# Kernel tuning notes

Hardware: AMD Instinct MI355X
Metric: run time of the kernel (lower is better)

## Reference

```python
import jax, jax.numpy as jnp
import numpy as np

B, N, V, E_PER = 64, 512, 64, 16384
IN, H, OUT = 128, 256, 10
TOTAL_N = B * N
E = B * E_PER


def _lin_init(key, fan_in, fan_out):
    return jax.random.normal(key, (fan_in, fan_out), jnp.float32) * (1.0 / np.sqrt(fan_in))


def setup_inputs() -> dict:
    key = jax.random.key(0)
    ks = jax.random.split(key, 16)
    x = jax.random.normal(ks[0], (TOTAL_N, IN), jnp.float32)
    # within-graph random edges, offset to global node ids
    off = (jnp.arange(B, dtype=jnp.int32) * N)[:, None]
    edge_src = (jax.random.randint(ks[1], (B, E_PER), 0, N, dtype=jnp.int32) + off).reshape(-1)
    edge_dst = (jax.random.randint(ks[2], (B, E_PER), 0, N, dtype=jnp.int32) + off).reshape(-1)
    inp = dict(
        x=x, edge_src=edge_src, edge_dst=edge_dst,
        W_emb=_lin_init(ks[3], IN, H), b_emb=jnp.zeros((H,), jnp.float32),
        W_gcn=_lin_init(ks[4], H, H), b_gcn=jnp.zeros((H,), jnp.float32),
        aW1=_lin_init(ks[5], H, H), ab1=jnp.zeros((H,), jnp.float32),
        aW2=_lin_init(ks[6], H, H), ab2=jnp.zeros((H,), jnp.float32),
        vW1=_lin_init(ks[7], H, H), vb1=jnp.zeros((H,), jnp.float32),
        vW2=_lin_init(ks[8], H, H), vb2=jnp.zeros((H,), jnp.float32),
        mW1=_lin_init(ks[9], H, H), mb1=jnp.zeros((H,), jnp.float32),
        mW2=_lin_init(ks[10], H, OUT), mb2=jnp.zeros((OUT,), jnp.float32),
        edge_weights=jnp.ones((B, N, V), jnp.float32) / V,  # uniform init
    )
    return inp


def reference(x, edge_src, edge_dst, W_emb, b_emb, W_gcn, b_gcn,
              aW1, ab1, aW2, ab2, vW1, vb1, vW2, vb2,
              mW1, mb1, mW2, mb2, edge_weights):
    # node embedding
    h = x @ W_emb + b_emb                                   # [BN, H]
    # GCNConv with symmetric normalization + self loops (PyG semantics)
    hw = h @ W_gcn                                          # [BN, H]
    deg = 1.0 + jax.ops.segment_sum(jnp.ones((E,), jnp.float32), edge_dst, num_segments=TOTAL_N)
    dinv = jax.lax.rsqrt(deg)
    coef = (dinv[edge_src] * dinv[edge_dst])[:, None]
    agg = jax.ops.segment_sum(hw[edge_src] * coef, edge_dst, num_segments=TOTAL_N)
    agg = agg + hw / deg[:, None]                           # self-loop term (norm = 1/deg)
    h = jax.nn.relu(agg + b_gcn)
    g = h.reshape(B, N, H)                                  # per-graph node features
    # affinity MLP + cosine similarity to graph prototype
    t = jax.nn.relu(g @ aW1 + ab1) @ aW2 + ab2              # [B, N, H]
    proto = t.mean(axis=1)                                  # [B, H]
    eps = 1e-8
    tn = jnp.maximum(jnp.linalg.norm(t, axis=-1), eps)      # [B, N]
    pn = jnp.maximum(jnp.linalg.norm(proto, axis=-1), eps)  # [B]
    sim = jnp.einsum('bnh,bh->bn', t, proto) / (tn * pn[:, None])
    att = 0.5 * (1.0 + sim)                                 # [B, N]
    mw = edge_weights * att[:, :, None]                     # [B, N, V]
    rs = mw.sum(axis=-1, keepdims=True)
    mw = mw / jnp.where(rs == 0.0, 1.0, rs)                 # row-normalize (top_k=None path)
    # weighted scatter of node features into virtual nodes
    vn = jnp.einsum('bnv,bnh->bvh', mw, g)                  # [B, V, H]
    vn = jax.nn.relu(vn @ vW1 + vb1) @ vW2 + vb2
    gf = vn.mean(axis=1)                                    # [B, H]
    out = jax.nn.relu(gf @ mW1 + mb1) @ mW2 + mb2           # [B, OUT]
    return out
```

## Files before the change

kernel.cpp:

```cpp
#include <hip/hip_runtime.h>
#include <hip/hip_bf16.h>

#define DEVINL __device__ __forceinline__

typedef unsigned short u16;
typedef short v8s   __attribute__((ext_vector_type(8)));
typedef float v4f   __attribute__((ext_vector_type(4)));
typedef u16   v4u16 __attribute__((ext_vector_type(4)));
typedef short v4s16 __attribute__((ext_vector_type(4)));

constexpr int Bg      = 64;
constexpr int Nn      = 512;
constexpr int Vv      = 64;
constexpr int IND     = 128;
constexpr int Hd      = 256;
constexpr int OUTD    = 10;
constexpr int TOTAL_N = Bg * Nn;
constexpr int NE      = Bg * 16384;
constexpr int E_PER   = 16384;

DEVINL u16 f2bf(float f) {
    unsigned u = __float_as_uint(f);
    u += 0x7FFF + ((u >> 16) & 1);
    return (u16)(u >> 16);
}
DEVINL float bf2f(u16 s) { return __uint_as_float(((unsigned)s) << 16); }

DEVINL void ld4f(const float* p, float o[4]) {
    float4 v = *(const float4*)p;
    o[0] = v.x; o[1] = v.y; o[2] = v.z; o[3] = v.w;
}
DEVINL void ld4f(const u16* p, float o[4]) {
    v4u16 v = *(const v4u16*)p;
    o[0] = bf2f(v[0]); o[1] = bf2f(v[1]); o[2] = bf2f(v[2]); o[3] = bf2f(v[3]);
}
DEVINL void stC(float* C, size_t idx, float v) { C[idx] = v; }
DEVINL void stC(u16* C, size_t idx, float v)   { C[idx] = f2bf(v); }

__global__ __launch_bounds__(1024) void k_csr(const int* __restrict__ esrc,
                                              const int* __restrict__ edst,
                                              int2* __restrict__ csr,
                                              int* __restrict__ rowstart,
                                              float* __restrict__ dinv) {
    __shared__ int   cnt[512];
    __shared__ int   cur[512];
    __shared__ float dv[512];
    int g = blockIdx.x;
    int tid = threadIdx.x;
    if (tid < 512) cnt[tid] = 0;
    __syncthreads();
    const int base = g * E_PER;
#pragma unroll
    for (int i = 0; i < E_PER / 1024; i++) {
        int d = edst[base + i * 1024 + tid];
        atomicAdd(&cnt[d & 511], 1);
    }
    __syncthreads();
    if (tid < 512) cur[tid] = cnt[tid];
    __syncthreads();
    for (int off = 1; off < 512; off <<= 1) {
        int v = 0;
        if (tid < 512 && tid >= off) v = cur[tid - off];
        __syncthreads();
        if (tid < 512) cur[tid] += v;
        __syncthreads();
    }
    if (tid < 512) {
        int excl = cur[tid] - cnt[tid];
        rowstart[g * 512 + tid] = base + excl;
        float di = rsqrtf((float)(cnt[tid] + 1));
        dv[tid] = di;
        dinv[g * 512 + tid] = di;
        cur[tid] = excl;
    }
    if (g == 0 && tid == 0) rowstart[TOTAL_N] = NE;
    __syncthreads();
#pragma unroll
    for (int i = 0; i < E_PER / 1024; i++) {
        int e = base + i * 1024 + tid;
        int s = esrc[e], d = edst[e];
        int sl = s & 511, dl = d & 511;
        int pos = atomicAdd(&cur[dl], 1);
        int2 rec;
        rec.x = s;
        rec.y = __float_as_int(dv[sl] * dv[dl]);
        csr[base + pos] = rec;
    }
}

struct WtArgs {
    const float* src[5];
    u16* dst[5];
};
__global__ __launch_bounds__(256) void k_wt(WtArgs a) {
    int bid = blockIdx.x;
    int mi = bid / 16, tile = bid % 16;
    int k0 = (tile & 3) * 64, n0 = (tile >> 2) * 64;
    const float* src = a.src[mi];
    u16* dst = a.dst[mi];
    __shared__ float T[64][65];
    int t = threadIdx.x;
#pragma unroll
    for (int j = 0; j < 16; j++) {
        int idx = t + 256 * j;
        int r = idx >> 6, c = idx & 63;
        T[c][r] = src[(size_t)(k0 + r) * 256 + n0 + c];
    }
    __syncthreads();
#pragma unroll
    for (int j = 0; j < 16; j++) {
        int idx = t + 256 * j;
        int nr = idx >> 6, kc = idx & 63;
        dst[(size_t)(n0 + nr) * 256 + k0 + kc] = f2bf(T[nr][kc]);
    }
}

__global__ __launch_bounds__(256) void k_b12(const float* __restrict__ b_emb,
                                             const float* __restrict__ W_gcn,
                                             float* __restrict__ b12) {
    int t = threadIdx.x;
    float acc = 0.f;
    for (int k = 0; k < IND; k++) acc += b_emb[k] * W_gcn[(size_t)k * 256 + t];
    b12[t] = acc;
}

template <typename TA, typename TC>
__global__ __launch_bounds__(256) void k_mfma_gemm(const TA* __restrict__ A,
                                                   const u16* __restrict__ Wt,
                                                   const float* __restrict__ bias,
                                                   const float* __restrict__ srow,
                                                   const float* __restrict__ b12v,
                                                   TC* __restrict__ C,
                                                   int M, int K, int relu, int tstore) {
    constexpr int LDK = 88;
    __shared__ short As[128 * LDK];
    __shared__ short Bs[128 * LDK];
    int tid  = threadIdx.x;
    int row0 = blockIdx.y * 128, col0 = blockIdx.x * 128;
    int lane = tid & 63, wid = tid >> 6;
    int wm = (wid >> 1) * 64, wn = (wid & 1) * 64;
    int q = lane >> 4, r = lane & 15;
    v4f acc[4][4];
#pragma unroll
    for (int i = 0; i < 4; i++)
#pragma unroll
        for (int j = 0; j < 4; j++) acc[i][j] = (v4f){0.f, 0.f, 0.f, 0.f};
    int sm = tid >> 1, sk = (tid & 1) * 32;
    for (int k0 = 0; k0 < K; k0 += 64) {
        const TA* ap  = A  + (size_t)(row0 + sm) * K + k0 + sk;
        const u16* bp = Wt + (size_t)(col0 + sm) * K + k0 + sk;
        short* adst = &As[sm * LDK + sk];
        short* bdst = &Bs[sm * LDK + sk];
#pragma unroll
        for (int i = 0; i < 8; i++) {
            float o[4];
            ld4f(ap + 4 * i, o);
            v4s16 pa;
            pa[0] = (short)f2bf(o[0]); pa[1] = (short)f2bf(o[1]);
            pa[2] = (short)f2bf(o[2]); pa[3] = (short)f2bf(o[3]);
            *(v4s16*)(adst + 4 * i) = pa;
            *(v4u16*)(bdst + 4 * i) = *(const v4u16*)(bp + 4 * i);
        }
        __syncthreads();
#pragma unroll
        for (int ks = 0; ks < 64; ks += 32) {
            v8s af[4], bfr[4];
#pragma unroll
            for (int i = 0; i < 4; i++)
                af[i] = *(const v8s*)&As[(wm + i * 16 + r) * LDK + ks + q * 8];
#pragma unroll
            for (int j = 0; j < 4; j++)
                bfr[j] = *(const v8s*)&Bs[(wn + j * 16 + r) * LDK + ks + q * 8];
#pragma unroll
            for (int i = 0; i < 4; i++)
#pragma unroll
                for (int j = 0; j < 4; j++)
                    acc[i][j] = __builtin_amdgcn_mfma_f32_16x16x32_bf16(af[i], bfr[j], acc[i][j], 0, 0, 0);
        }
        __syncthreads();
    }
#pragma unroll
    for (int i = 0; i < 4; i++) {
#pragma unroll
        for (int j = 0; j < 4; j++) {
            int col = col0 + wn + j * 16 + r;
            float bcol = bias ? bias[col] : 0.f;
            float b12c = b12v ? b12v[col] : 0.f;
#pragma unroll
            for (int rg = 0; rg < 4; rg++) {
                int row = row0 + wm + i * 16 + q * 4 + rg;
                float v = acc[i][j][rg] + bcol;
                if (srow) v += srow[row] * b12c;
                if (relu) v = fmaxf(v, 0.f);
                if (tstore) stC(C, (size_t)col * M + row, v);
                else        stC(C, (size_t)row * 256 + col, v);
            }
        }
    }
}

__global__ __launch_bounds__(128) void k_aggx(const float* __restrict__ x,
                                              const int* __restrict__ rowstart,
                                              const int2* __restrict__ csr,
                                              const float* __restrict__ dinv,
                                              float* __restrict__ xa,
                                              float* __restrict__ s) {
    __shared__ int2 lrec[128];
    int node = ((blockIdx.x & 7) << 12) | (blockIdx.x >> 3);
    int ch = threadIdx.x;
    float di = dinv[node];
    float invdeg = di * di;
    float acc = x[(size_t)node * IND + ch] * invdeg;
    float ssum = invdeg;
    int rs0 = rowstart[node], rs1 = rowstart[node + 1];
    for (int base = rs0; base < rs1; base += 128) {
        int e = base + ch;
        if (e < rs1) lrec[ch] = csr[e];
        __syncthreads();
        int m = min(128, rs1 - base);
        for (int i = 0; i < m; i++) {
            int2 rr = lrec[i];
            float c = __int_as_float(rr.y);
            acc += x[(size_t)rr.x * IND + ch] * c;
            ssum += c;
        }
        __syncthreads();
    }
    xa[(size_t)node * IND + ch] = acc;
    if (ch == 0) s[node] = ssum;
}

__global__ __launch_bounds__(1024) void k_proto(const u16* __restrict__ t,
                                                float* __restrict__ proto,
                                                float* __restrict__ pn) {
    __shared__ float part[4][256];
    __shared__ float red[256];
    int b = blockIdx.x;
    int tid = threadIdx.x;
    int st = tid >> 8, ch = tid & 255;
    float sm = 0.f;
    int n0 = st * 128;
    for (int n = n0; n < n0 + 128; n++)
        sm += bf2f(t[(size_t)(b * Nn + n) * Hd + ch]);
    part[st][ch] = sm;
    __syncthreads();
    if (tid < 256) {
        float p = (part[0][ch] + part[1][ch] + part[2][ch] + part[3][ch]) * (1.f / (float)Nn);
        proto[b * Hd + ch] = p;
        red[ch] = p * p;
    }
    __syncthreads();
    for (int off = 128; off > 0; off >>= 1) {
        if (tid < off) red[tid] += red[tid + off];
        __syncthreads();
    }
    if (tid == 0) pn[b] = fmaxf(sqrtf(red[0]), 1e-8f);
}

__global__ __launch_bounds__(256) void k_att(const u16* __restrict__ t,
                                             const float* __restrict__ proto,
                                             const float* __restrict__ pn,
                                             const float* __restrict__ ew,
                                             float* __restrict__ scale) {
    int tid = threadIdx.x;
    int lane = tid & 63, widx = tid >> 6;
    int node = blockIdx.x * 4 + widx;
    int b = node >> 9;
    v4u16 tv4 = *(const v4u16*)&t[(size_t)node * Hd + lane * 4];
    float4 pv4 = *(const float4*)&proto[b * Hd + lane * 4];
    float t0 = bf2f(tv4[0]), t1 = bf2f(tv4[1]), t2 = bf2f(tv4[2]), t3 = bf2f(tv4[3]);
    float dot = t0 * pv4.x + t1 * pv4.y + t2 * pv4.z + t3 * pv4.w;
    float sq  = t0 * t0 + t1 * t1 + t2 * t2 + t3 * t3;
    float wv  = ew[(size_t)node * Vv + lane];
#pragma unroll
    for (int off = 32; off > 0; off >>= 1) {
        dot += __shfl_xor(dot, off);
        sq  += __shfl_xor(sq, off);
        wv  += __shfl_xor(wv, off);
    }
    if (lane == 0) {
        float tn  = fmaxf(sqrtf(sq), 1e-8f);
        float sim = dot / (tn * pn[b]);
        float att = 0.5f * (1.f + sim);
        float rs  = att * wv;
        float den = (rs == 0.f) ? 1.f : rs;
        scale[node] = att / den;
    }
}

constexpr int LDV = 36;
DEVINL v8s ld_frag36(const short* p) {
    v4s16 lo = *(const v4s16*)p;
    v4s16 hi = *(const v4s16*)(p + 4);
    v8s f;
    f[0] = lo[0]; f[1] = lo[1]; f[2] = lo[2]; f[3] = lo[3];
    f[4] = hi[0]; f[5] = hi[1]; f[6] = hi[2]; f[7] = hi[3];
    return f;
}
__global__ __launch_bounds__(256) void k_vn_mfma(const float* __restrict__ ew,
                                                 const float* __restrict__ scale,
                                                 const u16* __restrict__ g,
                                                 u16* __restrict__ vn) {
    __shared__ short As[64 * LDV];
    __shared__ short Bs[256 * LDV];
    int b = blockIdx.x;
    int tid = threadIdx.x;
    int lane = tid & 63, wid = tid >> 6;
    int h0 = wid * 64;
    int q = lane >> 4, r = lane & 15;
    v4f acc[4][4];
#pragma unroll
    for (int i = 0; i < 4; i++)
#pragma unroll
        for (int j = 0; j < 4; j++) acc[i][j] = (v4f){0.f, 0.f, 0.f, 0.f};
    for (int k0 = 0; k0 < Nn; k0 += 32) {
#pragma unroll
        for (int p = 0; p < 8; p++) {
            int e = tid + 256 * p;
            int nl = e >> 6, v = e & 63;
            int n = b * Nn + k0 + nl;
            As[v * LDV + nl] = (short)f2bf(ew[(size_t)n * Vv + v] * scale[n]);
        }
#pragma unroll
        for (int p = 0; p < 8; p++) {
            int e = tid + 256 * p;
            int h = e & 255, kgrp = e >> 8;
            int kl = kgrp * 4;
            v4s16 tmp;
#pragma unroll
            for (int c = 0; c < 4; c++)
                tmp[c] = (short)g[(size_t)(b * Nn + k0 + kl + c) * Hd + h];
            *(v4s16*)&Bs[h * LDV + kl] = tmp;
        }
        __syncthreads();
        v8s af[4], bfr[4];
#pragma unroll
        for (int i = 0; i < 4; i++)
            af[i] = ld_frag36(&As[(i * 16 + r) * LDV + q * 8]);
#pragma unroll
        for (int j = 0; j < 4; j++)
            bfr[j] = ld_frag36(&Bs[(h0 + j * 16 + r) * LDV + q * 8]);
#pragma unroll
        for (int i = 0; i < 4; i++)
#pragma unroll
            for (int j = 0; j < 4; j++)
                acc[i][j] = __builtin_amdgcn_mfma_f32_16x16x32_bf16(af[i], bfr[j], acc[i][j], 0, 0, 0);
        __syncthreads();
    }
#pragma unroll
    for (int i = 0; i < 4; i++)
#pragma unroll
        for (int j = 0; j < 4; j++) {
            int col = h0 + j * 16 + r;
#pragma unroll
            for (int rg = 0; rg < 4; rg++) {
                int v = i * 16 + q * 4 + rg;
                vn[(size_t)(b * Vv + v) * Hd + col] = f2bf(acc[i][j][rg]);
            }
        }
}

__global__ __launch_bounds__(256) void k_head(const float* __restrict__ vn2,
                                              const float* __restrict__ mW1,
                                              const float* __restrict__ mb1,
                                              const float* __restrict__ mW2,
                                              const float* __restrict__ mb2,
                                              float* __restrict__ out) {
    __shared__ float gfs[256];
    __shared__ float zs[256];
    int b = blockIdx.x, t = threadIdx.x;
    float s = 0.f;
    for (int v = 0; v < Vv; v++) s += vn2[(size_t)(b * Vv + v) * Hd + t];
    gfs[t] = s * (1.f / (float)Vv);
    __syncthreads();
    float z = mb1[t];
    for (int k = 0; k < Hd; k++) z += gfs[k] * mW1[k * Hd + t];
    zs[t] = fmaxf(z, 0.f);
    __syncthreads();
    if (t < OUTD) {
        float o = mb2[t];
        for (int ch = 0; ch < Hd; ch++) o += zs[ch] * mW2[ch * OUTD + t];
        out[b * OUTD + t] = o;
    }
}

extern "C" void kernel_launch(void* const* d_in, const int* in_sizes, int n_in,
                              void* d_out, int out_size, void* d_ws, size_t ws_size,
                              hipStream_t stream) {
    const float* x     = (const float*)d_in[0];
    const int*   esrc  = (const int*)d_in[1];
    const int*   edst  = (const int*)d_in[2];
    const float* W_emb = (const float*)d_in[3];
    const float* b_emb = (const float*)d_in[4];
    const float* W_gcn = (const float*)d_in[5];
    const float* b_gcn = (const float*)d_in[6];
    const float* aW1   = (const float*)d_in[7];
    const float* ab1   = (const float*)d_in[8];
    const float* aW2   = (const float*)d_in[9];
    const float* ab2   = (const float*)d_in[10];
    const float* vW1   = (const float*)d_in[11];
    const float* vb1   = (const float*)d_in[12];
    const float* vW2   = (const float*)d_in[13];
    const float* vb2   = (const float*)d_in[14];
    const float* mW1   = (const float*)d_in[15];
    const float* mb1   = (const float*)d_in[16];
    const float* mW2   = (const float*)d_in[17];
    const float* mb2   = (const float*)d_in[18];
    const float* ew    = (const float*)d_in[19];
    float* out = (float*)d_out;

    char* w = (char*)d_ws;
    auto alloc = [&](size_t bytes) -> void* {
        void* p = (void*)w;
        w += (bytes + 255) & ~(size_t)255;
        return p;
    };
    int*   rowstart = (int*)  alloc((TOTAL_N + 1) * 4);
    float* dinv     = (float*)alloc(TOTAL_N * 4);
    int2*  csr      = (int2*) alloc((size_t)NE * 8);
    float* xa       = (float*)alloc((size_t)TOTAL_N * IND * 4);
    float* srow     = (float*)alloc(TOTAL_N * 4);
    u16*   g_bf     = (u16*)  alloc((size_t)TOTAL_N * Hd * 2);
    u16*   t1_bf    = (u16*)  alloc((size_t)TOTAL_N * Hd * 2);
    u16*   t_bf     = (u16*)  alloc((size_t)TOTAL_N * Hd * 2);
    u16*   vn_bf    = (u16*)  alloc((size_t)Bg * Vv * Hd * 2);
    u16*   vtmp_bf  = (u16*)  alloc((size_t)Bg * Vv * Hd * 2);
    float* vn2      = (float*)alloc((size_t)Bg * Vv * Hd * 4);
    float* proto    = (float*)alloc(Bg * Hd * 4);
    float* pn       = (float*)alloc(Bg * 4);
    float* scale    = (float*)alloc(TOTAL_N * 4);
    float* b12      = (float*)alloc(Hd * 4);
    u16*   wt_gcn   = (u16*)  alloc((size_t)Hd * Hd * 2);
    u16*   wt_a1    = (u16*)  alloc((size_t)Hd * Hd * 2);
    u16*   wt_a2    = (u16*)  alloc((size_t)Hd * Hd * 2);
    u16*   wt_v1    = (u16*)  alloc((size_t)Hd * Hd * 2);
    u16*   wt_v2    = (u16*)  alloc((size_t)Hd * Hd * 2);
    u16*   wt_12    = (u16*)  alloc((size_t)Hd * IND * 2);

    WtArgs wa;
    wa.src[0] = W_gcn; wa.dst[0] = wt_gcn;
    wa.src[1] = aW1;   wa.dst[1] = wt_a1;
    wa.src[2] = aW2;   wa.dst[2] = wt_a2;
    wa.src[3] = vW1;   wa.dst[3] = wt_v1;
    wa.src[4] = vW2;   wa.dst[4] = wt_v2;
    k_wt<<<80, 256, 0, stream>>>(wa);

    k_mfma_gemm<float, u16><<<dim3(2, 1), 256, 0, stream>>>(
        W_emb, wt_gcn, nullptr, nullptr, nullptr, wt_12, IND, Hd, 0, 1);
    k_b12<<<1, 256, 0, stream>>>(b_emb, W_gcn, b12);

    k_csr<<<Bg, 1024, 0, stream>>>(esrc, edst, csr, rowstart, dinv);

    k_aggx<<<TOTAL_N, 128, 0, stream>>>(x, rowstart, csr, dinv, xa, srow);

    k_mfma_gemm<float, u16><<<dim3(2, TOTAL_N / 128), 256, 0, stream>>>(
        xa, wt_12, b_gcn, srow, b12, g_bf, TOTAL_N, IND, 1, 0);

    k_mfma_gemm<u16, u16><<<dim3(2, TOTAL_N / 128), 256, 0, stream>>>(
        g_bf, wt_a1, ab1, nullptr, nullptr, t1_bf, TOTAL_N, Hd, 1, 0);
    k_mfma_gemm<u16, u16><<<dim3(2, TOTAL_N / 128), 256, 0, stream>>>(
        t1_bf, wt_a2, ab2, nullptr, nullptr, t_bf, TOTAL_N, Hd, 0, 0);

    k_proto<<<Bg, 1024, 0, stream>>>(t_bf, proto, pn);
    k_att<<<TOTAL_N / 4, 256, 0, stream>>>(t_bf, proto, pn, ew, scale);

    k_vn_mfma<<<Bg, 256, 0, stream>>>(ew, scale, g_bf, vn_bf);

    k_mfma_gemm<u16, u16><<<dim3(2, (Bg * Vv) / 128), 256, 0, stream>>>(
        vn_bf, wt_v1, vb1, nullptr, nullptr, vtmp_bf, Bg * Vv, Hd, 1, 0);
    k_mfma_gemm<u16, float><<<dim3(2, (Bg * Vv) / 128), 256, 0, stream>>>(
        vtmp_bf, wt_v2, vb2, nullptr, nullptr, vn2, Bg * Vv, Hd, 0, 0);

    k_head<<<Bg, 256, 0, stream>>>(vn2, mW1, mb1, mW2, mb2, out);
}
```

Measured before the change: 324.6 us.

## Split vn kernel across H, fold b12 and row sums, unroll reductions

k_vn_mfma now runs four blocks per graph, each covering a 64-column slice of H, which raises the block count from 64 to 256 to fill more CUs. The extra A-tile rebuild this causes is repeated in every block. The per-node coefficient row sum moves from k_aggx into k_csr through shared-memory float atomics, and k_csr loads edges as int4 and caches the destination ids in LDS. k_b12 is merged into k_wt as an extra block, which removes one launch. The k_aggx and k_proto inner loops use four independent accumulators to expose more memory-level parallelism, which changes floating-point summation order.

```diff
diff --git a/kernel.cpp b/kernel.cpp
--- a/kernel.cpp
+++ b/kernel.cpp
@@ -8,6 +8,7 @@
 typedef float v4f   __attribute__((ext_vector_type(4)));
 typedef u16   v4u16 __attribute__((ext_vector_type(4)));
 typedef short v4s16 __attribute__((ext_vector_type(4)));
+typedef int   v4i   __attribute__((ext_vector_type(4)));
 
 constexpr int Bg      = 64;
 constexpr int Nn      = 512;
@@ -41,19 +42,30 @@
                                               const int* __restrict__ edst,
                                               int2* __restrict__ csr,
                                               int* __restrict__ rowstart,
-                                              float* __restrict__ dinv) {
+                                              float* __restrict__ dinv,
+                                              float* __restrict__ srow) {
     __shared__ int   cnt[512];
     __shared__ int   cur[512];
     __shared__ float dv[512];
+    __shared__ float sfs[512];
+    __shared__ u16   dlc[E_PER];
     int g = blockIdx.x;
     int tid = threadIdx.x;
-    if (tid < 512) cnt[tid] = 0;
+    if (tid < 512) { cnt[tid] = 0; sfs[tid] = 0.f; }
     __syncthreads();
     const int base = g * E_PER;
-#pragma unroll
-    for (int i = 0; i < E_PER / 1024; i++) {
-        int d = edst[base + i * 1024 + tid];
-        atomicAdd(&cnt[d & 511], 1);
+    const v4i* edst4 = (const v4i*)(edst + base);
+    const v4i* esrc4 = (const v4i*)(esrc + base);
+#pragma unroll
+    for (int i = 0; i < E_PER / 4096; i++) {
+        int idx = i * 1024 + tid;
+        v4i d4 = edst4[idx];
+#pragma unroll
+        for (int c = 0; c < 4; c++) {
+            int dl = d4[c] & 511;
+            dlc[idx * 4 + c] = (u16)dl;
+            atomicAdd(&cnt[dl], 1);
+        }
     }
     __syncthreads();
     if (tid < 512) cur[tid] = cnt[tid];
@@ -76,30 +88,52 @@
     if (g == 0 && tid == 0) rowstart[TOTAL_N] = NE;
     __syncthreads();
 #pragma unroll
-    for (int i = 0; i < E_PER / 1024; i++) {
-        int e = base + i * 1024 + tid;
-        int s = esrc[e], d = edst[e];
-        int sl = s & 511, dl = d & 511;
-        int pos = atomicAdd(&cur[dl], 1);
-        int2 rec;
-        rec.x = s;
-        rec.y = __float_as_int(dv[sl] * dv[dl]);
-        csr[base + pos] = rec;
-    }
+    for (int i = 0; i < E_PER / 4096; i++) {
+        int idx = i * 1024 + tid;
+        v4i s4 = esrc4[idx];
+#pragma unroll
+        for (int c = 0; c < 4; c++) {
+            int s = s4[c];
+            int dl = dlc[idx * 4 + c];
+            float coef = dv[s & 511] * dv[dl];
+            int pos = atomicAdd(&cur[dl], 1);
+            int2 rec;
+            rec.x = s;
+            rec.y = __float_as_int(coef);
+            csr[base + pos] = rec;
+            atomicAdd(&sfs[dl], coef);
+        }
+    }
+    __syncthreads();
+    if (tid < 512) srow[g * 512 + tid] = sfs[tid] + dv[tid] * dv[tid];
 }
 
 struct WtArgs {
     const float* src[5];
     u16* dst[5];
+    const float* b_emb;
+    float* b12;
 };
 __global__ __launch_bounds__(256) void k_wt(WtArgs a) {
     int bid = blockIdx.x;
+    int t = threadIdx.x;
+    if (bid == 80) {
+        const float* Wg = a.src[0];
+        float a0 = 0.f, a1 = 0.f, a2 = 0.f, a3 = 0.f;
+        for (int k = 0; k < IND; k += 4) {
+            a0 += a.b_emb[k]     * Wg[(size_t)k * 256 + t];
+            a1 += a.b_emb[k + 1] * Wg[(size_t)(k + 1) * 256 + t];
+            a2 += a.b_emb[k + 2] * Wg[(size_t)(k + 2) * 256 + t];
+            a3 += a.b_emb[k + 3] * Wg[(size_t)(k + 3) * 256 + t];
+        }
+        a.b12[t] = (a0 + a1) + (a2 + a3);
+        return;
+    }
     int mi = bid / 16, tile = bid % 16;
     int k0 = (tile & 3) * 64, n0 = (tile >> 2) * 64;
     const float* src = a.src[mi];
     u16* dst = a.dst[mi];
     __shared__ float T[64][65];
-    int t = threadIdx.x;
 #pragma unroll
     for (int j = 0; j < 16; j++) {
         int idx = t + 256 * j;
@@ -113,15 +147,6 @@
         int nr = idx >> 6, kc = idx & 63;
         dst[(size_t)(n0 + nr) * 256 + k0 + kc] = f2bf(T[nr][kc]);
     }
-}
-
-__global__ __launch_bounds__(256) void k_b12(const float* __restrict__ b_emb,
-                                             const float* __restrict__ W_gcn,
-                                             float* __restrict__ b12) {
-    int t = threadIdx.x;
-    float acc = 0.f;
-    for (int k = 0; k < IND; k++) acc += b_emb[k] * W_gcn[(size_t)k * 256 + t];
-    b12[t] = acc;
 }
 
 template <typename TA, typename TC>
@@ -203,31 +228,35 @@
                                               const int* __restrict__ rowstart,
                                               const int2* __restrict__ csr,
                                               const float* __restrict__ dinv,
-                                              float* __restrict__ xa,
-                                              float* __restrict__ s) {
+                                              float* __restrict__ xa) {
     __shared__ int2 lrec[128];
     int node = ((blockIdx.x & 7) << 12) | (blockIdx.x >> 3);
     int ch = threadIdx.x;
     float di = dinv[node];
-    float invdeg = di * di;
-    float acc = x[(size_t)node * IND + ch] * invdeg;
-    float ssum = invdeg;
+    float acc = x[(size_t)node * IND + ch] * (di * di);
     int rs0 = rowstart[node], rs1 = rowstart[node + 1];
     for (int base = rs0; base < rs1; base += 128) {
         int e = base + ch;
         if (e < rs1) lrec[ch] = csr[e];
         __syncthreads();
         int m = min(128, rs1 - base);
-        for (int i = 0; i < m; i++) {
+        float a0 = 0.f, a1 = 0.f, a2 = 0.f, a3 = 0.f;
+        int i = 0;
+        for (; i + 4 <= m; i += 4) {
+            int2 r0 = lrec[i], r1 = lrec[i + 1], r2 = lrec[i + 2], r3 = lrec[i + 3];
+            a0 += x[(size_t)r0.x * IND + ch] * __int_as_float(r0.y);
+            a1 += x[(size_t)r1.x * IND + ch] * __int_as_float(r1.y);
+            a2 += x[(size_t)r2.x * IND + ch] * __int_as_float(r2.y);
+            a3 += x[(size_t)r3.x * IND + ch] * __int_as_float(r3.y);
+        }
+        for (; i < m; i++) {
             int2 rr = lrec[i];
-            float c = __int_as_float(rr.y);
-            acc += x[(size_t)rr.x * IND + ch] * c;
-            ssum += c;
-        }
+            a0 += x[(size_t)rr.x * IND + ch] * __int_as_float(rr.y);
+        }
+        acc += (a0 + a1) + (a2 + a3);
         __syncthreads();
     }
     xa[(size_t)node * IND + ch] = acc;
-    if (ch == 0) s[node] = ssum;
 }
 
 __global__ __launch_bounds__(1024) void k_proto(const u16* __restrict__ t,
@@ -238,11 +267,15 @@
     int b = blockIdx.x;
     int tid = threadIdx.x;
     int st = tid >> 8, ch = tid & 255;
-    float sm = 0.f;
     int n0 = st * 128;
-    for (int n = n0; n < n0 + 128; n++)
-        sm += bf2f(t[(size_t)(b * Nn + n) * Hd + ch]);
-    part[st][ch] = sm;
+    float s0 = 0.f, s1 = 0.f, s2 = 0.f, s3 = 0.f;
+    for (int n = n0; n < n0 + 128; n += 4) {
+        s0 += bf2f(t[(size_t)(b * Nn + n)     * Hd + ch]);
+        s1 += bf2f(t[(size_t)(b * Nn + n + 1) * Hd + ch]);
+        s2 += bf2f(t[(size_t)(b * Nn + n + 2) * Hd + ch]);
+        s3 += bf2f(t[(size_t)(b * Nn + n + 3) * Hd + ch]);
+    }
+    part[st][ch] = (s0 + s1) + (s2 + s3);
     __syncthreads();
     if (tid < 256) {
         float p = (part[0][ch] + part[1][ch] + part[2][ch] + part[3][ch]) * (1.f / (float)Nn);
@@ -302,17 +335,18 @@
                                                  const u16* __restrict__ g,
                                                  u16* __restrict__ vn) {
     __shared__ short As[64 * LDV];
-    __shared__ short Bs[256 * LDV];
-    int b = blockIdx.x;
+    __shared__ short Bs[64 * LDV];
+    int bid = blockIdx.x;
+    int b = bid >> 2, h0 = (bid & 3) * 64;
     int tid = threadIdx.x;
     int lane = tid & 63, wid = tid >> 6;
-    int h0 = wid * 64;
+    int wm = (wid >> 1) * 32, wn = (wid & 1) * 32;
     int q = lane >> 4, r = lane & 15;
-    v4f acc[4][4];
-#pragma unroll
-    for (int i = 0; i < 4; i++)
-#pragma unroll
-        for (int j = 0; j < 4; j++) acc[i][j] = (v4f){0.f, 0.f, 0.f, 0.f};
+    v4f acc[2][2];
+#pragma unroll
+    for (int i = 0; i < 2; i++)
+#pragma unroll
+        for (int j = 0; j < 2; j++) acc[i][j] = (v4f){0.f, 0.f, 0.f, 0.f};
     for (int k0 = 0; k0 < Nn; k0 += 32) {
 #pragma unroll
         for (int p = 0; p < 8; p++) {
@@ -322,39 +356,39 @@
             As[v * LDV + nl] = (short)f2bf(ew[(size_t)n * Vv + v] * scale[n]);
         }
 #pragma unroll
-        for (int p = 0; p < 8; p++) {
+        for (int p = 0; p < 2; p++) {
             int e = tid + 256 * p;
-            int h = e & 255, kgrp = e >> 8;
+            int hl = e & 63, kgrp = e >> 6;
             int kl = kgrp * 4;
             v4s16 tmp;
 #pragma unroll
             for (int c = 0; c < 4; c++)
-                tmp[c] = (short)g[(size_t)(b * Nn + k0 + kl + c) * Hd + h];
-            *(v4s16*)&Bs[h * LDV + kl] = tmp;
-        }
-        __syncthreads();
-        v8s af[4], bfr[4];
-#pragma unroll
-        for (int i = 0; i < 4; i++)
-            af[i] = ld_frag36(&As[(i * 16 + r) * LDV + q * 8]);
-#pragma unroll
-        for (int j = 0; j < 4; j++)
-            bfr[j] = ld_frag36(&Bs[(h0 + j * 16 + r) * LDV + q * 8]);
-#pragma unroll
-        for (int i = 0; i < 4; i++)
-#pragma unroll
-            for (int j = 0; j < 4; j++)
+                tmp[c] = (short)g[(size_t)(b * Nn + k0 + kl + c) * Hd + h0 + hl];
+            *(v4s16*)&Bs[hl * LDV + kl] = tmp;
+        }
+        __syncthreads();
+        v8s af[2], bfr[2];
+#pragma unroll
+        for (int i = 0; i < 2; i++)
+            af[i] = ld_frag36(&As[(wm + i * 16 + r) * LDV + q * 8]);
+#pragma unroll
+        for (int j = 0; j < 2; j++)
+            bfr[j] = ld_frag36(&Bs[(wn + j * 16 + r) * LDV + q * 8]);
+#pragma unroll
+        for (int i = 0; i < 2; i++)
+#pragma unroll
+            for (int j = 0; j < 2; j++)
                 acc[i][j] = __builtin_amdgcn_mfma_f32_16x16x32_bf16(af[i], bfr[j], acc[i][j], 0, 0, 0);
         __syncthreads();
     }
 #pragma unroll
-    for (int i = 0; i < 4; i++)
-#pragma unroll
-        for (int j = 0; j < 4; j++) {
-            int col = h0 + j * 16 + r;
+    for (int i = 0; i < 2; i++)
+#pragma unroll
+        for (int j = 0; j < 2; j++) {
+            int col = h0 + wn + j * 16 + r;
 #pragma unroll
             for (int rg = 0; rg < 4; rg++) {
-                int v = i * 16 + q * 4 + rg;
+                int v = wm + i * 16 + q * 4 + rg;
                 vn[(size_t)(b * Vv + v) * Hd + col] = f2bf(acc[i][j][rg]);
             }
         }
@@ -443,15 +477,15 @@
     wa.src[2] = aW2;   wa.dst[2] = wt_a2;
     wa.src[3] = vW1;   wa.dst[3] = wt_v1;
     wa.src[4] = vW2;   wa.dst[4] = wt_v2;
-    k_wt<<<80, 256, 0, stream>>>(wa);
+    wa.b_emb = b_emb;  wa.b12 = b12;
+    k_wt<<<81, 256, 0, stream>>>(wa);
 
     k_mfma_gemm<float, u16><<<dim3(2, 1), 256, 0, stream>>>(
         W_emb, wt_gcn, nullptr, nullptr, nullptr, wt_12, IND, Hd, 0, 1);
-    k_b12<<<1, 256, 0, stream>>>(b_emb, W_gcn, b12);
-
-    k_csr<<<Bg, 1024, 0, stream>>>(esrc, edst, csr, rowstart, dinv);
-
-    k_aggx<<<TOTAL_N, 128, 0, stream>>>(x, rowstart, csr, dinv, xa, srow);
+
+    k_csr<<<Bg, 1024, 0, stream>>>(esrc, edst, csr, rowstart, dinv, srow);
+
+    k_aggx<<<TOTAL_N, 128, 0, stream>>>(x, rowstart, csr, dinv, xa);
 
     k_mfma_gemm<float, u16><<<dim3(2, TOTAL_N / 128), 256, 0, stream>>>(
         xa, wt_12, b_gcn, srow, b12, g_bf, TOTAL_N, IND, 1, 0);
@@ -464,7 +498,7 @@
     k_proto<<<Bg, 1024, 0, stream>>>(t_bf, proto, pn);
     k_att<<<TOTAL_N / 4, 256, 0, stream>>>(t_bf, proto, pn, ew, scale);
 
-    k_vn_mfma<<<Bg, 256, 0, stream>>>(ew, scale, g_bf, vn_bf);
+    k_vn_mfma<<<Bg * 4, 256, 0, stream>>>(ew, scale, g_bf, vn_bf);
 
     k_mfma_gemm<u16, u16><<<dim3(2, (Bg * Vv) / 128), 256, 0, stream>>>(
         vn_bf, wt_v1, vb1, nullptr, nullptr, vtmp_bf, Bg * Vv, Hd, 1, 0);
```

Measured after the change: 357.0 us. 10.0% more time.
